# Kernel optimization log

Measured on AMD Instinct MI355X. Metric: run time of the kernel, lower is better.

Reference implementation:

```python
import jax, jax.numpy as jnp
import numpy as np

IN_DIM, D, B, N = 6, 256, 2048, 100  # inner_dim=latent_dim=256, max_size=100


def _glorot(key, shape):
    fan = sum(shape)
    return jax.random.uniform(key, shape, jnp.float32, -1.0, 1.0) * np.sqrt(6.0 / fan)


def setup_inputs() -> dict:
    key = jax.random.key(0)
    ks = jax.random.split(key, 16)
    inp = {
        "x": jax.random.normal(ks[0], (B, N, IN_DIM), jnp.float32),
        "full": 1,
        "remap_w": _glorot(ks[1], (D, IN_DIM)),
        "remap_b": jnp.zeros((D,), jnp.float32),
    }
    for l in range(4):
        k = jax.random.split(ks[2 + l], 3)
        inp[f"w{l+1}"] = _glorot(k[0], (D, D))          # GATConv lin weight (bias=False)
        inp[f"as{l+1}"] = _glorot(k[1], (D,)) * 0.1      # att_src
        inp[f"ad{l+1}"] = _glorot(k[2], (D,)) * 0.1      # att_dst
        inp[f"b{l+1}"] = jnp.zeros((D,), jnp.float32)    # post-aggregation bias
    return inp


def _gat(h, w, a_src, a_dst, b):
    # Complete digraph with self-loops (full=True path) => dense softmax attention.
    g = jnp.einsum("bnd,od->bno", h, w)                  # [B,N,D] transformed nodes
    s_src = jnp.einsum("bno,o->bn", g, a_src)            # score of node as source j
    s_dst = jnp.einsum("bno,o->bn", g, a_dst)            # score of node as target i
    logits = jax.nn.leaky_relu(s_dst[:, :, None] + s_src[:, None, :], 0.2)  # [B,i,j]
    attn = jax.nn.softmax(logits, axis=-1)               # softmax over sources per target
    return jnp.einsum("bij,bjo->bio", attn, g) + b


def reference(x, full, remap_w, remap_b,
              w1, as1, ad1, b1, w2, as2, ad2, b2,
              w3, as3, ad3, b3, w4, as4, ad4, b4):
    h = jax.nn.relu(jnp.einsum("bni,oi->bno", x, remap_w) + remap_b)
    h = jax.nn.relu(_gat(h, w1, as1, ad1, b1) + h)
    h = jax.nn.relu(_gat(h, w2, as2, ad2, b2) + h)
    h = jax.nn.relu(_gat(h, w3, as3, ad3, b3) + h)
    h = _gat(h, w4, as4, ad4, b4)
    return h
```

## Files before the change

kernel.cpp:

```cpp
#include <hip/hip_runtime.h>
#include <hip/hip_bf16.h>


typedef __attribute__((ext_vector_type(8)))  short bf16x8;
typedef __attribute__((ext_vector_type(4)))  short bf16x4;
typedef __attribute__((ext_vector_type(4)))  float f32x4;
typedef __attribute__((ext_vector_type(16))) float f32x16;

__device__ __forceinline__ float bf2f(unsigned short u) {
    return __uint_as_float(((unsigned)u) << 16);
}
__device__ __forceinline__ short f2bfs(float f) {
    __hip_bfloat16 h = __float2bfloat16(f);
    return *reinterpret_cast<short*>(&h);
}

#define HS_OFF 0
#define GT_OFF 51200
#define P_OFF  116736
#define SS_OFF 149504
#define SD_OFF 150016
#define SMEM_BYTES 150528

__device__ __forceinline__ int hs_addr(int row, int col) {
    return HS_OFF + row * 512 + ((col * 2) ^ ((row & 7) << 4));
}
__device__ __forceinline__ int gt_addr(int o, int n) {
    return GT_OFF + o * 256 + ((n * 2) ^ ((o & 7) << 4));
}
__device__ __forceinline__ int p_addr(int i, int j) {
    return P_OFF + i * 256 + ((j * 2) ^ ((i & 7) << 4));
}

struct LayerPtrs {
    const float* w[4];
    const float* bias[4];
};
struct PrepPtrs {
    const float* w[4];
    const float* as_[4];
    const float* ad_[4];
};

__global__ __launch_bounds__(256) void prep_kernel(PrepPtrs p, unsigned short* wsd) {
    const int l = blockIdx.x;
    const int d = threadIdx.x;
    __shared__ float As[256], Ad[256];
    As[d] = p.as_[l][d];
    Ad[d] = p.ad_[l][d];
    __syncthreads();
    const float* W = p.w[l];
    float s1 = 0.f, s2 = 0.f;
    for (int o = 0; o < 256; ++o) {
        float wv = W[o * 256 + d];
        s1 = fmaf(wv, As[o], s1);
        s2 = fmaf(wv, Ad[o], s2);
    }
    wsd[l * 512 + d]       = (unsigned short)f2bfs(s1);
    wsd[l * 512 + 256 + d] = (unsigned short)f2bfs(s2);
}

__global__ __launch_bounds__(64) void prep_wfrag_kernel(PrepPtrs p, unsigned short* wbf2) {
    const int bid  = blockIdx.x;
    const int l    = bid >> 7;
    const int nt   = (bid >> 4) & 7;
    const int ks   = bid & 15;
    const int lane = threadIdx.x;
    const int o    = nt * 32 + (lane & 31);
    const int kb   = ks * 16 + (lane >> 5) * 8;
    const float* W = p.w[l];
    bf16x8 v;
#pragma unroll
    for (int e = 0; e < 8; ++e) v[e] = f2bfs(W[o * 256 + kb + e]);
    *(bf16x8*)(wbf2 + ((size_t)bid * 64 + lane) * 8) = v;
}

__global__ __launch_bounds__(1024) void geom_kernel(
    const float* __restrict__ x,
    const float* __restrict__ remap_w,
    const float* __restrict__ remap_b,
    LayerPtrs lp,
    const unsigned short* __restrict__ wsd,
    const unsigned short* __restrict__ wbf2,
    float* __restrict__ out)
{
    extern __shared__ char smem[];
    const int tid  = threadIdx.x;
    const int lane = tid & 63;
    const int wv   = tid >> 6;
    const int hi   = lane >> 5;
    const int ln   = lane & 31;
    const int mt   = wv >> 2;
    const int np   = wv & 3;
    const int b    = blockIdx.x;

    const int o0 = np * 64 + ln;
    const int o1 = o0 + 32;

    {
        const int o = tid & 255, quarter = tid >> 8;
        float rw[6];
#pragma unroll
        for (int i = 0; i < 6; ++i) rw[i] = remap_w[o * 6 + i];
        const float rb = remap_b[o];
        const float* xb = x + (size_t)b * 600;
        for (int n = quarter * 25; n < quarter * 25 + 25; ++n) {
            float v = rb;
#pragma unroll
            for (int i = 0; i < 6; ++i) v = fmaf(xb[n * 6 + i], rw[i], v);
            v = fmaxf(v, 0.f);
            *(unsigned short*)(smem + hs_addr(n, o)) = (unsigned short)f2bfs(v);
        }
    }

    for (int l = 0; l < 4; ++l) {
        __syncthreads();

        {
            f32x16 acc0, acc1, accS;
#pragma unroll
            for (int i = 0; i < 16; ++i) { acc0[i] = 0.f; acc1[i] = 0.f; accS[i] = 0.f; }
            int arow = mt * 32 + ln;
            if (arow > 99) arow = 99;
#pragma unroll
            for (int ks = 0; ks < 16; ++ks) {
                bf16x8 a = *(const bf16x8*)(smem + hs_addr(arow, ks * 16 + hi * 8));
                bf16x8 b0, b1;
                if (wbf2) {
                    const unsigned short* wp =
                        wbf2 + (((size_t)(l * 8 + 2 * np) * 16 + ks) * 64 + lane) * 8;
                    b0 = *(const bf16x8*)(wp);
                    b1 = *(const bf16x8*)(wp + 16 * 64 * 8);
                } else {
                    const float* W = lp.w[l];
#pragma unroll
                    for (int e = 0; e < 8; ++e) {
                        b0[e] = f2bfs(W[o0 * 256 + ks * 16 + hi * 8 + e]);
                        b1[e] = f2bfs(W[o1 * 256 + ks * 16 + hi * 8 + e]);
                    }
                }
                acc0 = __builtin_amdgcn_mfma_f32_32x32x16_bf16(a, b0, acc0, 0, 0, 0);
                acc1 = __builtin_amdgcn_mfma_f32_32x32x16_bf16(a, b1, acc1, 0, 0, 0);
                if (np == 0) {
                    const unsigned short* wsp = wsd + l * 512 + ks * 16 + hi * 8;
                    bf16x8 bs = *(const bf16x8*)(wsp);
                    bf16x8 bd = *(const bf16x8*)(wsp + 256);
                    bf16x8 bz = {0, 0, 0, 0, 0, 0, 0, 0};
                    bf16x8 bb = (ln == 0) ? bs : ((ln == 1) ? bd : bz);
                    accS = __builtin_amdgcn_mfma_f32_32x32x16_bf16(a, bb, accS, 0, 0, 0);
                }
            }
#pragma unroll
            for (int g4 = 0; g4 < 4; ++g4) {
                bf16x4 v0, v1;
#pragma unroll
                for (int jj = 0; jj < 4; ++jj) {
                    v0[jj] = f2bfs(acc0[g4 * 4 + jj]);
                    v1[jj] = f2bfs(acc1[g4 * 4 + jj]);
                }
                const int node = mt * 32 + 8 * g4 + 4 * hi;
                *(bf16x4*)(smem + gt_addr(o0, node)) = v0;
                *(bf16x4*)(smem + gt_addr(o1, node)) = v1;
            }
            if (np == 0 && ln < 2) {
                float* dst = (float*)(smem + (ln == 0 ? SS_OFF : SD_OFF));
#pragma unroll
                for (int reg = 0; reg < 16; ++reg) {
                    const int row = mt * 32 + (reg & 3) + 8 * (reg >> 2) + 4 * hi;
                    if (row < 100) dst[row] = accS[reg];
                }
            }
        }
        __syncthreads();

        {
            const int i = tid >> 3, s3 = tid & 7;
            if (i < 100) {
                const float sd = ((float*)(smem + SD_OFF))[i];
                const float* Ssf = (const float*)(smem + SS_OFF);
                float vals[2][8];
                float mx = -1e30f;
#pragma unroll
                for (int t = 0; t < 2; ++t) {
                    const int blk = t * 8 + s3;
#pragma unroll
                    for (int e = 0; e < 8; ++e) {
                        const int j = blk * 8 + e;
                        float v;
                        if (j < 100) {
                            float z = sd + Ssf[j];
                            v = (z > 0.f) ? z : 0.2f * z;
                        } else {
                            v = -1e30f;
                        }
                        vals[t][e] = v;
                        mx = fmaxf(mx, v);
                    }
                }
                mx = fmaxf(mx, __shfl_xor(mx, 1, 8));
                mx = fmaxf(mx, __shfl_xor(mx, 2, 8));
                mx = fmaxf(mx, __shfl_xor(mx, 4, 8));
                float sum = 0.f;
#pragma unroll
                for (int t = 0; t < 2; ++t)
#pragma unroll
                    for (int e = 0; e < 8; ++e) {
                        float ev = __expf(vals[t][e] - mx);
                        vals[t][e] = ev;
                        sum += ev;
                    }
                sum += __shfl_xor(sum, 1, 8);
                sum += __shfl_xor(sum, 2, 8);
                sum += __shfl_xor(sum, 4, 8);
                const float inv = 1.f / sum;
#pragma unroll
                for (int t = 0; t < 2; ++t) {
                    const int blk = t * 8 + s3;
                    bf16x8 pv;
#pragma unroll
                    for (int e = 0; e < 8; ++e) pv[e] = f2bfs(vals[t][e] * inv);
                    *(bf16x8*)(smem + p_addr(i, blk * 8)) = pv;
                }
            } else {
                bf16x8 z = {0, 0, 0, 0, 0, 0, 0, 0};
#pragma unroll
                for (int t = 0; t < 2; ++t)
                    *(bf16x8*)(smem + p_addr(i, (t * 8 + s3) * 8)) = z;
            }
        }
        __syncthreads();

        {
            f32x16 c0, c1;
#pragma unroll
            for (int i = 0; i < 16; ++i) { c0[i] = 0.f; c1[i] = 0.f; }
            const int prow = mt * 32 + ln;
#pragma unroll
            for (int ks = 0; ks < 8; ++ks) {
                bf16x8 a  = *(const bf16x8*)(smem + p_addr(prow, ks * 16 + hi * 8));
                bf16x8 b0 = *(const bf16x8*)(smem + gt_addr(o0, ks * 16 + hi * 8));
                bf16x8 b1 = *(const bf16x8*)(smem + gt_addr(o1, ks * 16 + hi * 8));
                c0 = __builtin_amdgcn_mfma_f32_32x32x16_bf16(a, b0, c0, 0, 0, 0);
                c1 = __builtin_amdgcn_mfma_f32_32x32x16_bf16(a, b1, c1, 0, 0, 0);
            }
            const float bia0 = lp.bias[l][o0];
            const float bia1 = lp.bias[l][o1];
            if (l < 3) {
#pragma unroll
                for (int reg = 0; reg < 16; ++reg) {
                    const int row = mt * 32 + (reg & 3) + 8 * (reg >> 2) + 4 * hi;
                    if (row < 100) {
                        {
                            const int ad = hs_addr(row, o0);
                            float r = bf2f(*(unsigned short*)(smem + ad));
                            *(unsigned short*)(smem + ad) =
                                (unsigned short)f2bfs(fmaxf(c0[reg] + bia0 + r, 0.f));
                        }
                        {
                            const int ad = hs_addr(row, o1);
                            float r = bf2f(*(unsigned short*)(smem + ad));
                            *(unsigned short*)(smem + ad) =
                                (unsigned short)f2bfs(fmaxf(c1[reg] + bia1 + r, 0.f));
                        }
                    }
                }
            } else {
                float* ob = out + (size_t)b * 25600;
#pragma unroll
                for (int reg = 0; reg < 16; ++reg) {
                    const int row = mt * 32 + (reg & 3) + 8 * (reg >> 2) + 4 * hi;
                    if (row < 100) {
                        ob[row * 256 + o0] = c0[reg] + bia0;
                        ob[row * 256 + o1] = c1[reg] + bia1;
                    }
                }
            }
        }
    }
}

extern "C" void kernel_launch(void* const* d_in, const int* in_sizes, int n_in,
                              void* d_out, int out_size, void* d_ws, size_t ws_size,
                              hipStream_t stream) {
    const float* x       = (const float*)d_in[0];
    const float* remap_w = (const float*)d_in[2];
    const float* remap_b = (const float*)d_in[3];
    PrepPtrs pp;
    LayerPtrs lp;
    for (int l = 0; l < 4; ++l) {
        lp.w[l]    = pp.w[l]   = (const float*)d_in[4 + 4 * l];
        pp.as_[l]  = (const float*)d_in[5 + 4 * l];
        pp.ad_[l]  = (const float*)d_in[6 + 4 * l];
        lp.bias[l] = (const float*)d_in[7 + 4 * l];
    }
    unsigned short* wsd = (unsigned short*)d_ws;
    unsigned short* wbf2 = nullptr;
    if (ws_size >= (size_t)(4096 + 4 * 65536 * 2)) {
        wbf2 = (unsigned short*)((char*)d_ws + 4096);
    }

    prep_kernel<<<4, 256, 0, stream>>>(pp, wsd);
    if (wbf2) prep_wfrag_kernel<<<512, 64, 0, stream>>>(pp, wbf2);

    (void)hipFuncSetAttribute(reinterpret_cast<const void*>(geom_kernel),
                              hipFuncAttributeMaxDynamicSharedMemorySize, SMEM_BYTES);
    geom_kernel<<<2048, 1024, SMEM_BYTES, stream>>>(x, remap_w, remap_b, lp, wsd, wbf2,
                                                    (float*)d_out);
}
```

Before: 775.6 us.

## Split dual-accumulator MFMA loops into sequential passes and widen LDS swizzles

Each wave's two 32-column output tiles are now computed one after the other instead of interleaved, in both the node-transform GEMM and the attention-aggregation GEMM. This halves the live accumulator registers, so 1024-thread blocks are less likely to spill. The cost is that the A operand is reloaded from LDS for the second tile and there is less independent MFMA work to hide latency. The LDS XOR swizzles are widened from 3 bits to 4 or 5 bits to cut bank conflicts, and the weight-fragment branch becomes a template parameter so the runtime check is removed from the inner loop.

```diff
diff --git a/kernel.cpp b/kernel.cpp
--- a/kernel.cpp
+++ b/kernel.cpp
@@ -23,13 +23,13 @@
 #define SMEM_BYTES 150528
 
 __device__ __forceinline__ int hs_addr(int row, int col) {
-    return HS_OFF + row * 512 + ((col * 2) ^ ((row & 7) << 4));
+    return HS_OFF + row * 512 + ((col * 2) ^ ((row & 31) << 4));
 }
 __device__ __forceinline__ int gt_addr(int o, int n) {
-    return GT_OFF + o * 256 + ((n * 2) ^ ((o & 7) << 4));
+    return GT_OFF + o * 256 + ((n * 2) ^ ((o & 15) << 4));
 }
 __device__ __forceinline__ int p_addr(int i, int j) {
-    return P_OFF + i * 256 + ((j * 2) ^ ((i & 7) << 4));
+    return P_OFF + i * 256 + ((j * 2) ^ ((i & 15) << 4));
 }
 
 struct LayerPtrs {
@@ -75,6 +75,7 @@
     *(bf16x8*)(wbf2 + ((size_t)bid * 64 + lane) * 8) = v;
 }
 
+template <bool USE_WBF2>
 __global__ __launch_bounds__(1024) void geom_kernel(
     const float* __restrict__ x,
     const float* __restrict__ remap_w,
@@ -94,9 +95,6 @@
     const int np   = wv & 3;
     const int b    = blockIdx.x;
 
-    const int o0 = np * 64 + ln;
-    const int o1 = o0 + 32;
-
     {
         const int o = tid & 255, quarter = tid >> 8;
         float rw[6];
@@ -116,31 +114,28 @@
     for (int l = 0; l < 4; ++l) {
         __syncthreads();
 
+        int arow = mt * 32 + ln;
+        if (arow > 99) arow = 99;
+
         {
-            f32x16 acc0, acc1, accS;
-#pragma unroll
-            for (int i = 0; i < 16; ++i) { acc0[i] = 0.f; acc1[i] = 0.f; accS[i] = 0.f; }
-            int arow = mt * 32 + ln;
-            if (arow > 99) arow = 99;
-#pragma unroll
+            const int o0 = np * 64 + ln;
+            f32x16 acc, accS;
+#pragma unroll
+            for (int i = 0; i < 16; ++i) { acc[i] = 0.f; accS[i] = 0.f; }
+#pragma unroll 4
             for (int ks = 0; ks < 16; ++ks) {
                 bf16x8 a = *(const bf16x8*)(smem + hs_addr(arow, ks * 16 + hi * 8));
-                bf16x8 b0, b1;
-                if (wbf2) {
-                    const unsigned short* wp =
-                        wbf2 + (((size_t)(l * 8 + 2 * np) * 16 + ks) * 64 + lane) * 8;
-                    b0 = *(const bf16x8*)(wp);
-                    b1 = *(const bf16x8*)(wp + 16 * 64 * 8);
+                bf16x8 b0;
+                if (USE_WBF2) {
+                    b0 = *(const bf16x8*)(wbf2 +
+                        (((size_t)(l * 8 + 2 * np) * 16 + ks) * 64 + lane) * 8);
                 } else {
                     const float* W = lp.w[l];
 #pragma unroll
-                    for (int e = 0; e < 8; ++e) {
+                    for (int e = 0; e < 8; ++e)
                         b0[e] = f2bfs(W[o0 * 256 + ks * 16 + hi * 8 + e]);
-                        b1[e] = f2bfs(W[o1 * 256 + ks * 16 + hi * 8 + e]);
-                    }
-                }
-                acc0 = __builtin_amdgcn_mfma_f32_32x32x16_bf16(a, b0, acc0, 0, 0, 0);
-                acc1 = __builtin_amdgcn_mfma_f32_32x32x16_bf16(a, b1, acc1, 0, 0, 0);
+                }
+                acc = __builtin_amdgcn_mfma_f32_32x32x16_bf16(a, b0, acc, 0, 0, 0);
                 if (np == 0) {
                     const unsigned short* wsp = wsd + l * 512 + ks * 16 + hi * 8;
                     bf16x8 bs = *(const bf16x8*)(wsp);
@@ -152,15 +147,10 @@
             }
 #pragma unroll
             for (int g4 = 0; g4 < 4; ++g4) {
-                bf16x4 v0, v1;
-#pragma unroll
-                for (int jj = 0; jj < 4; ++jj) {
-                    v0[jj] = f2bfs(acc0[g4 * 4 + jj]);
-                    v1[jj] = f2bfs(acc1[g4 * 4 + jj]);
-                }
-                const int node = mt * 32 + 8 * g4 + 4 * hi;
-                *(bf16x4*)(smem + gt_addr(o0, node)) = v0;
-                *(bf16x4*)(smem + gt_addr(o1, node)) = v1;
+                bf16x4 v0;
+#pragma unroll
+                for (int jj = 0; jj < 4; ++jj) v0[jj] = f2bfs(acc[g4 * 4 + jj]);
+                *(bf16x4*)(smem + gt_addr(o0, mt * 32 + 8 * g4 + 4 * hi)) = v0;
             }
             if (np == 0 && ln < 2) {
                 float* dst = (float*)(smem + (ln == 0 ? SS_OFF : SD_OFF));
@@ -169,6 +159,34 @@
                     const int row = mt * 32 + (reg & 3) + 8 * (reg >> 2) + 4 * hi;
                     if (row < 100) dst[row] = accS[reg];
                 }
+            }
+        }
+        {
+            const int o1 = np * 64 + 32 + ln;
+            f32x16 acc;
+#pragma unroll
+            for (int i = 0; i < 16; ++i) acc[i] = 0.f;
+#pragma unroll 4
+            for (int ks = 0; ks < 16; ++ks) {
+                bf16x8 a = *(const bf16x8*)(smem + hs_addr(arow, ks * 16 + hi * 8));
+                bf16x8 b1;
+                if (USE_WBF2) {
+                    b1 = *(const bf16x8*)(wbf2 +
+                        (((size_t)(l * 8 + 2 * np + 1) * 16 + ks) * 64 + lane) * 8);
+                } else {
+                    const float* W = lp.w[l];
+#pragma unroll
+                    for (int e = 0; e < 8; ++e)
+                        b1[e] = f2bfs(W[o1 * 256 + ks * 16 + hi * 8 + e]);
+                }
+                acc = __builtin_amdgcn_mfma_f32_32x32x16_bf16(a, b1, acc, 0, 0, 0);
+            }
+#pragma unroll
+            for (int g4 = 0; g4 < 4; ++g4) {
+                bf16x4 v1;
+#pragma unroll
+                for (int jj = 0; jj < 4; ++jj) v1[jj] = f2bfs(acc[g4 * 4 + jj]);
+                *(bf16x4*)(smem + gt_addr(o1, mt * 32 + 8 * g4 + 4 * hi)) = v1;
             }
         }
         __syncthreads();
@@ -230,38 +248,29 @@
         }
         __syncthreads();
 
-        {
-            f32x16 c0, c1;
-#pragma unroll
-            for (int i = 0; i < 16; ++i) { c0[i] = 0.f; c1[i] = 0.f; }
-            const int prow = mt * 32 + ln;
-#pragma unroll
+        const int prow = mt * 32 + ln;
+#pragma unroll
+        for (int t = 0; t < 2; ++t) {
+            const int o = np * 64 + t * 32 + ln;
+            f32x16 c;
+#pragma unroll
+            for (int i = 0; i < 16; ++i) c[i] = 0.f;
+#pragma unroll 4
             for (int ks = 0; ks < 8; ++ks) {
                 bf16x8 a  = *(const bf16x8*)(smem + p_addr(prow, ks * 16 + hi * 8));
-                bf16x8 b0 = *(const bf16x8*)(smem + gt_addr(o0, ks * 16 + hi * 8));
-                bf16x8 b1 = *(const bf16x8*)(smem + gt_addr(o1, ks * 16 + hi * 8));
-                c0 = __builtin_amdgcn_mfma_f32_32x32x16_bf16(a, b0, c0, 0, 0, 0);
-                c1 = __builtin_amdgcn_mfma_f32_32x32x16_bf16(a, b1, c1, 0, 0, 0);
-            }
-            const float bia0 = lp.bias[l][o0];
-            const float bia1 = lp.bias[l][o1];
+                bf16x8 bg = *(const bf16x8*)(smem + gt_addr(o, ks * 16 + hi * 8));
+                c = __builtin_amdgcn_mfma_f32_32x32x16_bf16(a, bg, c, 0, 0, 0);
+            }
+            const float bia = lp.bias[l][o];
             if (l < 3) {
 #pragma unroll
                 for (int reg = 0; reg < 16; ++reg) {
                     const int row = mt * 32 + (reg & 3) + 8 * (reg >> 2) + 4 * hi;
                     if (row < 100) {
-                        {
-                            const int ad = hs_addr(row, o0);
-                            float r = bf2f(*(unsigned short*)(smem + ad));
-                            *(unsigned short*)(smem + ad) =
-                                (unsigned short)f2bfs(fmaxf(c0[reg] + bia0 + r, 0.f));
-                        }
-                        {
-                            const int ad = hs_addr(row, o1);
-                            float r = bf2f(*(unsigned short*)(smem + ad));
-                            *(unsigned short*)(smem + ad) =
-                                (unsigned short)f2bfs(fmaxf(c1[reg] + bia1 + r, 0.f));
-                        }
+                        const int ad = hs_addr(row, o);
+                        float r = bf2f(*(unsigned short*)(smem + ad));
+                        *(unsigned short*)(smem + ad) =
+                            (unsigned short)f2bfs(fmaxf(c[reg] + bia + r, 0.f));
                     }
                 }
             } else {
@@ -269,10 +278,7 @@
 #pragma unroll
                 for (int reg = 0; reg < 16; ++reg) {
                     const int row = mt * 32 + (reg & 3) + 8 * (reg >> 2) + 4 * hi;
-                    if (row < 100) {
-                        ob[row * 256 + o0] = c0[reg] + bia0;
-                        ob[row * 256 + o1] = c1[reg] + bia1;
-                    }
+                    if (row < 100) ob[row * 256 + o] = c[reg] + bia;
                 }
             }
         }
@@ -300,10 +306,17 @@
     }
 
     prep_kernel<<<4, 256, 0, stream>>>(pp, wsd);
-    if (wbf2) prep_wfrag_kernel<<<512, 64, 0, stream>>>(pp, wbf2);
-
-    (void)hipFuncSetAttribute(reinterpret_cast<const void*>(geom_kernel),
-                              hipFuncAttributeMaxDynamicSharedMemorySize, SMEM_BYTES);
-    geom_kernel<<<2048, 1024, SMEM_BYTES, stream>>>(x, remap_w, remap_b, lp, wsd, wbf2,
-                                                    (float*)d_out);
-}
+
+    if (wbf2) {
+        prep_wfrag_kernel<<<512, 64, 0, stream>>>(pp, wbf2);
+        (void)hipFuncSetAttribute(reinterpret_cast<const void*>(geom_kernel<true>),
+                                  hipFuncAttributeMaxDynamicSharedMemorySize, SMEM_BYTES);
+        geom_kernel<true><<<2048, 1024, SMEM_BYTES, stream>>>(x, remap_w, remap_b, lp,
+                                                              wsd, wbf2, (float*)d_out);
+    } else {
+        (void)hipFuncSetAttribute(reinterpret_cast<const void*>(geom_kernel<false>),
+                                  hipFuncAttributeMaxDynamicSharedMemorySize, SMEM_BYTES);
+        geom_kernel<false><<<2048, 1024, SMEM_BYTES, stream>>>(x, remap_w, remap_b, lp,
+                                                               wsd, wbf2, (float*)d_out);
+    }
+}
```

Result: slower. 841.3 us (+8.5%).
